# Kernel optimization log

Hardware: AMD Instinct MI355X
Metric: run time of the kernel (lower is better)

Reference implementation:

```python
import jax, jax.numpy as jnp
import numpy as np

EMB_DIM = 64
TREE_DIM = 128
VOCAB = 10000
SORT_VOCAB = 64
DEPTH = 8  # levels 0..8; leaves are level 0, root is level DEPTH
N_TREES = 256


def _tree_topology(depth):
    # perfect binary tree, nodes laid out leaves-first so the root is the LAST node
    level_sizes = [2 ** (depth - l) for l in range(depth + 1)]
    offsets = np.cumsum([0] + level_sizes)
    n = int(offsets[-1])  # 2^(depth+1)-1
    node_order = np.concatenate([np.full(level_sizes[l], l, np.int64) for l in range(depth + 1)])
    par, chi, eo = [], [], []
    for l in range(1, depth + 1):
        p = offsets[l] + np.arange(level_sizes[l])
        c0 = offsets[l - 1] + 2 * np.arange(level_sizes[l])
        par.append(np.repeat(p, 2))
        chi.append(np.stack([c0, c0 + 1], 1).reshape(-1))
        eo.append(np.full(2 * level_sizes[l], l, np.int64))
    return n, node_order, np.concatenate(par), np.concatenate(chi), np.concatenate(eo)


def setup_inputs():
    key = jax.random.key(0)
    ks = jax.random.split(key, 16)
    n, no, par, chi, eo = _tree_topology(DEPTH)
    offs = np.arange(N_TREES, dtype=np.int64) * n
    node_order = jnp.asarray(np.tile(no, N_TREES))
    parent_idx = jnp.asarray((par[None, :] + offs[:, None]).reshape(-1))
    child_idx = jnp.asarray((chi[None, :] + offs[:, None]).reshape(-1))
    edge_order = jnp.asarray(np.tile(eo, N_TREES))
    NT = N_TREES * n
    in_dim = 3 * EMB_DIM  # token_emb | sort_emb | const_emb

    def nrm(k, shape, s=0.05):
        return jax.random.normal(k, shape, jnp.float32) * s

    return dict(
        tokens_a=jax.random.randint(ks[0], (NT,), 0, VOCAB * 2),
        sorts_a=jax.random.randint(ks[1], (NT,), 0, SORT_VOCAB * 2),
        const_a=nrm(ks[2], (NT, EMB_DIM), 1.0),
        tokens_b=jax.random.randint(ks[3], (NT,), 0, VOCAB * 2),
        sorts_b=jax.random.randint(ks[4], (NT,), 0, SORT_VOCAB * 2),
        const_b=nrm(ks[5], (NT, EMB_DIM), 1.0),
        node_order=node_order, parent_idx=parent_idx, child_idx=child_idx,
        edge_order=edge_order, n_levels=DEPTH + 1, n_trees=N_TREES,
        emb=nrm(ks[6], (VOCAB * 2, EMB_DIM), 1.0),
        sort_emb_tab=nrm(ks[7], (SORT_VOCAB * 2, EMB_DIM), 1.0),
        W_iou=nrm(ks[8], (in_dim, 3 * TREE_DIM)),
        b_iou=jnp.zeros((3 * TREE_DIM,), jnp.float32),
        U_iou=nrm(ks[9], (TREE_DIM, 3 * TREE_DIM)),
        W_f=nrm(ks[10], (in_dim, TREE_DIM)),
        b_f=jnp.zeros((TREE_DIM,), jnp.float32),
        U_f=nrm(ks[11], (TREE_DIM, TREE_DIM)),
        fc1_w=nrm(ks[12], (2 * TREE_DIM + 1, TREE_DIM)),
        fc1_b=jnp.zeros((TREE_DIM,), jnp.float32),
        fc2_w=nrm(ks[13], (TREE_DIM, 2)),
        fc2_b=jnp.zeros((2,), jnp.float32),
    )


def _treelstm(feat, node_order, parent_idx, child_idx, edge_order, n_levels,
              W_iou, b_iou, U_iou, W_f, b_f, U_f):
    # child-sum TreeLSTM, level-synchronous from leaves (level 0) to root.
    N = feat.shape[0]
    td = U_f.shape[0]
    h = jnp.zeros((N, td), feat.dtype)
    c = jnp.zeros((N, td), feat.dtype)
    wiou_x = feat @ W_iou + b_iou  # [N, 3*td], hoisted out of the level loop
    wf_x = feat @ W_f + b_f        # [N, td]
    for t in range(n_levels):
        nmask = (node_order == t)[:, None]
        emask = (edge_order == t)[:, None].astype(feat.dtype)
        ch = h[child_idx]  # [E, td]
        cc = c[child_idx]
        h_sum = jax.ops.segment_sum(ch * emask, parent_idx, num_segments=N)
        f = jax.nn.sigmoid(wf_x[parent_idx] + ch @ U_f)  # per-edge forget gate
        c_sum = jax.ops.segment_sum(f * cc * emask, parent_idx, num_segments=N)
        i, o, u = jnp.split(wiou_x + h_sum @ U_iou, 3, axis=1)
        c_new = jax.nn.sigmoid(i) * jnp.tanh(u) + c_sum
        h_new = jax.nn.sigmoid(o) * jnp.tanh(c_new)
        h = jnp.where(nmask, h_new, h)
        c = jnp.where(nmask, c_new, c)
    return h, c


def reference(tokens_a, sorts_a, const_a, tokens_b, sorts_b, const_b,
              node_order, parent_idx, child_idx, edge_order, n_levels, n_trees,
              emb, sort_emb_tab, W_iou, b_iou, U_iou, W_f, b_f, U_f,
              fc1_w, fc1_b, fc2_w, fc2_b):
    def tree_root_h(tokens, sorts, const):
        feat = jnp.concatenate([emb[tokens], sort_emb_tab[sorts], const], axis=1)
        h, _ = _treelstm(feat, node_order, parent_idx, child_idx, edge_order,
                         n_levels, W_iou, b_iou, U_iou, W_f, b_f, U_f)
        n_per = h.shape[0] // n_trees
        roots = jnp.arange(n_trees) * n_per + (n_per - 1)  # stack_last_h: root is last node
        return h[roots]
    ha = tree_root_h(tokens_a, sorts_a, const_a)  # [B, td]
    hb = tree_root_h(tokens_b, sorts_b, const_b)
    dotp = jnp.sum(ha * hb, axis=-1, keepdims=True)  # diag(ha @ hb.T)
    hcat = jnp.concatenate([ha, hb, dotp], axis=-1)  # [B, 2*td+1]
    logits = jax.nn.relu(hcat @ fc1_w + fc1_b) @ fc2_w + fc2_b  # [B, 2]
    return logits
```

## Files before the change

kernel.cpp:

```cpp
#include <hip/hip_runtime.h>
#include <stdint.h>
#include <stddef.h>

typedef unsigned short u16;
typedef unsigned long long u64;
typedef short bf16x8 __attribute__((ext_vector_type(8)));
typedef float f32x4 __attribute__((ext_vector_type(4)));

#define NTREES 256
#define NPT 511
#define TD 128
#define PLANE_E ((size_t)65536 * TD)

#define S_TOKA 0
#define S_SRTA 1
#define S_CSTA 2
#define S_TOKB 3
#define S_SRTB 4
#define S_CSTB 5
#define S_EMB  6
#define S_SORT 7
#define S_WIOU 8
#define S_BIOU 9
#define S_UIOU 10
#define S_WF   11
#define S_BF   12
#define S_UF   13
#define S_W1   14
#define S_B1   15
#define S_W2   16
#define S_B2   17

#define O_WIOU 0
#define O_WF   73728
#define O_UIOU 98304
#define O_UF   147456
#define O_BIOU 163840
#define O_BF   164224
#define O_W1   164352
#define O_B1   197248
#define O_W2   197376
#define O_B2   197632
#define W_TOTAL 197634

struct ArgPack { u64 p[32]; int sz[32]; int n; };

static __device__ __forceinline__ float bf2f(u16 x){
  union { unsigned u; float f; } v; v.u = ((unsigned)x) << 16; return v.f;
}
static __device__ __forceinline__ u16 f2bf(float f){
  union { float f; unsigned u; } v; v.f = f;
  unsigned r = v.u + 0x7fffu + ((v.u >> 16) & 1u);
  return (u16)(r >> 16);
}
static __device__ __forceinline__ float sigm(float x){ return 1.f/(1.f+expf(-x)); }
static __device__ __forceinline__ float ldin(const void* p, size_t i, int fl){
  return fl ? ((const float*)p)[i] : bf2f(((const u16*)p)[i]);
}
static __device__ __forceinline__ int ldint(const void* p, size_t i, int i64){
  return ((const int*)p)[i << i64];
}

__global__ void resolve_k(ArgPack ap, u64* __restrict__ tab, int* __restrict__ flags){
  if (threadIdx.x != 0 || blockIdx.x != 0) return;
  if (ap.n >= 24) {
    const int map[18] = {0,1,2,3,4,5,12,13,14,15,16,17,18,19,20,21,22,23};
    for (int s = 0; s < 18; ++s) tab[s] = ap.p[map[s]];
  } else if (ap.n >= 22) {
    const int map[18] = {0,1,2,3,4,5,10,11,12,13,14,15,16,17,18,19,20,21};
    for (int s = 0; s < 18; ++s) tab[s] = ap.p[map[s]];
  }
  int ntok = 0, nsrt = 0, ncst = 0, nb128 = 0;
  int tok_i64 = 0, srt_i64 = 0;
  for (int i = 0; i < ap.n && i < 32; ++i) {
    const int s = ap.sz[i];
    const u64 p = ap.p[i];
    int slot = -1;
    if (s == 8372224)      { slot = ncst ? S_CSTB : S_CSTA; ncst++; }
    else if (s == 130816) {
      const int* q = (const int*)p;
      int nz = 0;
      for (int j = 300; j < 430; ++j) if (q[2 * j + 1] != 0) nz++;
      const int w = (nz == 0) ? 1 : 0;
      long vmax = 0;
      for (int j = 256; j < 768; ++j) { long v = w ? (long)q[2 * j] : (long)q[j]; if (v > vmax) vmax = v; }
      if (vmax <= 16)        slot = -1;
      else if (vmax <= 4096) { slot = nsrt ? S_SRTB : S_SRTA; nsrt++; srt_i64 = w; }
      else                   { slot = ntok ? S_TOKB : S_TOKA; ntok++; tok_i64 = w; }
    }
    else if (s == 1280000) slot = S_EMB;
    else if (s == 8192)    slot = S_SORT;
    else if (s == 73728)   slot = S_WIOU;
    else if (s == 384)     slot = S_BIOU;
    else if (s == 49152)   slot = S_UIOU;
    else if (s == 24576)   slot = S_WF;
    else if (s == 128)     { slot = nb128 ? S_B1 : S_BF; nb128++; }
    else if (s == 16384)   slot = S_UF;
    else if (s == 32896)   slot = S_W1;
    else if (s == 256)     slot = S_W2;
    else if (s == 2)       slot = S_B2;
    if (slot >= 0) tab[slot] = p;
  }
  flags[1] = tok_i64;
  flags[2] = srt_i64;
  const u16* pu = (const u16*)tab[S_EMB];
  int huge = 0;
  for (int i = 0; i < 1024; ++i) { const float v = fabsf(bf2f(pu[2 * i])); if (v > 1e4f) huge++; }
  flags[0] = (huge > 40) ? 1 : 0;
}

__global__ __launch_bounds__(256) void prep_k(const u64* __restrict__ tab,
    const int* __restrict__ flags, float* __restrict__ wf)
{
  const int fl = flags[0];
  const int tid = blockIdx.x * 256 + threadIdx.x;
  if (tid >= W_TOTAL) return;
  float v;
  if      (tid < O_WF)   v = ldin((const void*)tab[S_WIOU], tid - O_WIOU, fl);
  else if (tid < O_UIOU) v = ldin((const void*)tab[S_WF],   tid - O_WF,   fl);
  else if (tid < O_UF)   v = ldin((const void*)tab[S_UIOU], tid - O_UIOU, fl);
  else if (tid < O_BIOU) v = ldin((const void*)tab[S_UF],   tid - O_UF,   fl);
  else if (tid < O_BF)   v = ldin((const void*)tab[S_BIOU], tid - O_BIOU, fl);
  else if (tid < O_W1)   v = ldin((const void*)tab[S_BF],   tid - O_BF,   fl);
  else if (tid < O_B1)   v = ldin((const void*)tab[S_W1],   tid - O_W1,   fl);
  else if (tid < O_W2)   v = ldin((const void*)tab[S_B1],   tid - O_B1,   fl);
  else if (tid < O_B2)   v = ldin((const void*)tab[S_W2],   tid - O_W2,   fl);
  else                   v = ldin((const void*)tab[S_B2],   tid - O_B2,   fl);
  wf[tid] = v;
}

__global__ __launch_bounds__(256) void prep_w(const u64* __restrict__ tab,
    const int* __restrict__ flags, u16* __restrict__ wzhi, u16* __restrict__ wzlo,
    float* __restrict__ bz)
{
  const int fl = flags[0];
  const int tid = blockIdx.x * 256 + threadIdx.x;
  if (tid < 640) {
    bz[tid] = (tid < 384) ? ldin((const void*)tab[S_BIOU], tid, fl)
                          : ldin((const void*)tab[S_BF], (tid - 384) & 127, fl);
  }
  if (tid >= 640 * 448) return;
  const int n = tid / 448, k = tid - n * 448;
  float v;
  if (k < 192) {
    v = (n < 384) ? ldin((const void*)tab[S_WIOU], (size_t)k * 384 + n, fl)
                  : ldin((const void*)tab[S_WF],   (size_t)k * 128 + ((n - 384) & 127), fl);
  } else if (k < 320) {
    const int kk = k - 192;
    v = (n < 384) ? ldin((const void*)tab[S_UIOU], (size_t)kk * 384 + n, fl)
      : (n < 512) ? ldin((const void*)tab[S_UF],   (size_t)kk * 128 + (n - 384), fl) : 0.f;
  } else {
    const int kk = k - 320;
    v = (n < 384) ? ldin((const void*)tab[S_UIOU], (size_t)kk * 384 + n, fl)
      : (n < 512) ? 0.f : ldin((const void*)tab[S_UF], (size_t)kk * 128 + (n - 512), fl);
  }
  const u16 hi = f2bf(v);
  wzhi[(size_t)n * 448 + k] = hi;
  wzlo[(size_t)n * 448 + k] = f2bf(v - bf2f(hi));
}

template<bool LEAF>
__global__ __launch_bounds__(512) void gemm_level_k(
    const u64* __restrict__ tab, const int* __restrict__ flags,
    const u16* __restrict__ wzhi, const u16* __restrict__ wzlo,
    const float* __restrict__ bz,
    u16* __restrict__ hhi, u16* __restrict__ hlo, float* __restrict__ cc,
    const int T, const int soArg, const int slotPerSide)
{
  constexpr int NKS = LEAF ? 6 : 14;
  constexpr int NG  = LEAF ? 3 : 5;
  __shared__ __align__(16) u16 Ah[2][4][64][8];
  __shared__ __align__(16) u16 Al[2][4][64][8];

  const int so = soArg + 3 * blockIdx.y;
  const size_t sb = (size_t)slotPerSide * blockIdx.y * TD;
  u16* hps = hhi + sb;
  u16* lps = hlo + sb;
  float* cps = cc + sb;
  const void* tokens = (const void*)tab[so + 0];
  const void* sorts  = (const void*)tab[so + 1];
  const void* cstp   = (const void*)tab[so + 2];
  const void* emb    = (const void*)tab[S_EMB];
  const void* sortt  = (const void*)tab[S_SORT];
  const int fl = flags[0], ti = flags[1], si = flags[2];
  const int tid = threadIdx.x, l = tid & 63, w = tid >> 6, lr = l & 15, lq = l >> 4;
  const int m0 = blockIdx.x * 64;
  const int lpt = 8 - T, mask = (1 << lpt) - 1, offp = 512 - (1 << (9 - T));

  const int srow = tid & 63, skq = tid >> 6;
  const int sm = m0 + srow;
  const int stree = sm >> lpt, sj = sm & mask;
  const size_t snode = (size_t)stree * NPT + offp + sj;
  int tok = ldint(tokens, snode, ti); tok = tok < 0 ? 0 : (tok > 19999 ? 19999 : tok);
  int srt = ldint(sorts,  snode, si); srt = srt < 0 ? 0 : (srt > 127 ? 127 : srt);
  size_t sc0 = 0, sc1 = 0;
  if (!LEAF) { sc0 = ((size_t)sm) << T; sc1 = sc0 + ((size_t)1 << (T - 1)); }

  auto stage = [&](int ks, int buf) {
    const int kg = ks * 32 + skq * 4;
    u16 hi4[4], lo4[4];
    if (LEAF || kg < 192) {
      if (fl) {
        const float* src;
        if (kg < 64)       src = (const float*)emb   + (size_t)tok * 64 + kg;
        else if (kg < 128) src = (const float*)sortt + (size_t)srt * 64 + (kg - 64);
        else               src = (const float*)cstp  + snode * 64 + (kg - 128);
        const float4 v = *(const float4*)src;
        const float xv[4] = {v.x, v.y, v.z, v.w};
#pragma unroll
        for (int j = 0; j < 4; ++j) {
          hi4[j] = f2bf(xv[j]);
          lo4[j] = f2bf(xv[j] - bf2f(hi4[j]));
        }
      } else {
        const u16* src;
        if (kg < 64)       src = (const u16*)emb   + (size_t)tok * 64 + kg;
        else if (kg < 128) src = (const u16*)sortt + (size_t)srt * 64 + (kg - 64);
        else               src = (const u16*)cstp  + snode * 64 + (kg - 128);
#pragma unroll
        for (int j = 0; j < 4; ++j) { hi4[j] = src[j]; lo4[j] = 0; }
      }
    } else {
      const size_t cslot = (kg < 320) ? sc0 : sc1;
      const int off = (kg < 320) ? (kg - 192) : (kg - 320);
      *(uint2*)hi4 = *(const uint2*)(hps + cslot * TD + off);
      *(uint2*)lo4 = *(const uint2*)(lps + cslot * TD + off);
    }
    *(uint2*)&Ah[buf][skq >> 1][srow][(skq & 1) * 4] = *(const uint2*)hi4;
    *(uint2*)&Al[buf][skq >> 1][srow][(skq & 1) * 4] = *(const uint2*)lo4;
  };

  f32x4 acc[4][NG];
#pragma unroll
  for (int mf = 0; mf < 4; ++mf)
#pragma unroll
    for (int g = 0; g < NG; ++g) acc[mf][g] = f32x4{0.f, 0.f, 0.f, 0.f};

  stage(0, 0);
  for (int ks = 0; ks < NKS; ++ks) {
    __syncthreads();
    if (ks + 1 < NKS) stage(ks + 1, (ks + 1) & 1);
    const int k0 = ks * 32;
    const int buf = ks & 1;
    bf16x8 ah[4], al[4];
#pragma unroll
    for (int mf = 0; mf < 4; ++mf) {
      ah[mf] = *(const bf16x8*)&Ah[buf][lq][mf * 16 + lr][0];
      al[mf] = *(const bf16x8*)&Al[buf][lq][mf * 16 + lr][0];
    }
#pragma unroll
    for (int g = 0; g < NG; ++g) {
      if (!LEAF) {
        if (g == 3 && k0 >= 320) continue;
        if (g == 4 && k0 >= 192 && k0 < 320) continue;
      }
      const size_t boff = (size_t)((g * 8 + w) * 16 + lr) * 448 + k0 + lq * 8;
      const bf16x8 bh = *(const bf16x8*)&wzhi[boff];
      const bf16x8 bl = *(const bf16x8*)&wzlo[boff];
#pragma unroll
      for (int mf = 0; mf < 4; ++mf) {
        acc[mf][g] = __builtin_amdgcn_mfma_f32_16x16x32_bf16(ah[mf], bh, acc[mf][g], 0, 0, 0);
        acc[mf][g] = __builtin_amdgcn_mfma_f32_16x16x32_bf16(al[mf], bh, acc[mf][g], 0, 0, 0);
        acc[mf][g] = __builtin_amdgcn_mfma_f32_16x16x32_bf16(ah[mf], bl, acc[mf][g], 0, 0, 0);
      }
    }
  }

  const int d = w * 16 + lr;
  const float bi = bz[d], bo = bz[128 + d], bu = bz[256 + d];
  float bf0 = 0.f, bf1 = 0.f;
  if (!LEAF) { bf0 = bz[384 + d]; bf1 = bz[512 + d]; }
#pragma unroll
  for (int mf = 0; mf < 4; ++mf) {
#pragma unroll
    for (int rr = 0; rr < 4; ++rr) {
      const int row = mf * 16 + lq * 4 + rr;
      const int m = m0 + row;
      const size_t ps = LEAF ? (size_t)m : (((size_t)m) << T);
      const float iv = acc[mf][0][rr] + bi;
      const float ov = acc[mf][1][rr] + bo;
      const float uv = acc[mf][2][rr] + bu;
      float cn = sigm(iv) * tanhf(uv);
      if (!LEAF) {
        const size_t c1s = ps + ((size_t)1 << (T - 1));
        cn += sigm(acc[mf][3][rr] + bf0) * cps[ps * TD + d]
            + sigm(acc[mf][4][rr] + bf1) * cps[c1s * TD + d];
      }
      cps[ps * TD + d] = cn;
      const float hv = sigm(ov) * tanhf(cn);
      const u16 hh = f2bf(hv);
      hps[ps * TD + d] = hh;
      lps[ps * TD + d] = f2bf(hv - bf2f(hh));
    }
  }
}

template<int L>
__global__ __launch_bounds__(128) void bottom_k(const u64* __restrict__ tab,
    const int* __restrict__ flags, const float* __restrict__ wf,
    float* __restrict__ h, float* __restrict__ c, const int so)
{
  constexpr int G = 16 >> L;
  __shared__ float sfeat[16][192];
  __shared__ float childh[16][128];
  const void* tokens = (const void*)tab[so + 0];
  const void* sorts  = (const void*)tab[so + 1];
  const void* cst    = (const void*)tab[so + 2];
  const void* emb    = (const void*)tab[S_EMB];
  const void* sortt  = (const void*)tab[S_SORT];
  const int d = threadIdx.x;
  const int fl = flags[0], ti = flags[1], si = flags[2];
  const int m0 = blockIdx.x * G;

  const float bi  = wf[O_BIOU + d];
  const float bo  = wf[O_BIOU + 128 + d];
  const float bu  = wf[O_BIOU + 256 + d];
  const float bf_ = wf[O_BF + d];

  for (int idx = d; idx < 16 * 192; idx += 128) {
    const int g = idx / 192, k = idx - g * 192;
    const int gl = (m0 << L) + g;
    const int tree = gl >> 8, j = gl & 255;
    const size_t node = (size_t)tree * NPT + j;
    float v;
    if (k < 64) {
      int tk = ldint(tokens, node, ti); tk = tk < 0 ? 0 : (tk > 19999 ? 19999 : tk);
      v = ldin(emb, (size_t)tk * 64 + k, fl);
    } else if (k < 128) {
      int sr = ldint(sorts, node, si); sr = sr < 0 ? 0 : (sr > 127 ? 127 : sr);
      v = ldin(sortt, (size_t)sr * 64 + (k - 64), fl);
    } else v = ldin(cst, node * 64 + (k - 128), fl);
    sfeat[g][k] = v;
  }
  __syncthreads();

  float hb[16], cb[16];
  {
    float ai[16], ao[16], au[16];
#pragma unroll
    for (int g = 0; g < 16; ++g) { ai[g] = bi; ao[g] = bo; au[g] = bu; }
    for (int k = 0; k < 192; ++k) {
      const float wi = wf[O_WIOU + (size_t)k * 384 + d];
      const float wo = wf[O_WIOU + (size_t)k * 384 + 128 + d];
      const float wu = wf[O_WIOU + (size_t)k * 384 + 256 + d];
#pragma unroll
      for (int g = 0; g < 16; ++g) {
        const float x = sfeat[g][k];
        ai[g] = fmaf(x, wi, ai[g]);
        ao[g] = fmaf(x, wo, ao[g]);
        au[g] = fmaf(x, wu, au[g]);
      }
    }
#pragma unroll
    for (int g = 0; g < 16; ++g) {
      const float cv = sigm(ai[g]) * tanhf(au[g]);
      cb[g] = cv;
      hb[g] = sigm(ao[g]) * tanhf(cv);
    }
  }

#pragma unroll
  for (int lev = 1; lev <= L; ++lev) {
    const int nn = 16 >> lev;
    __syncthreads();
#pragma unroll
    for (int j = 0; j < 32; ++j)
      if (j < 2 * nn) childh[j][d] = hb[j];
    for (int idx = d; idx < nn * 192; idx += 128) {
      const int g = idx / 192, k = idx - g * 192;
      const int gle = (m0 << (L - lev)) + g;
      const int lpt = 8 - lev;
      const int tree = gle >> lpt, j = gle & ((1 << lpt) - 1);
      const size_t node = (size_t)tree * NPT + (512 - (1 << (9 - lev))) + j;
      float v;
      if (k < 64) {
        int tk = ldint(tokens, node, ti); tk = tk < 0 ? 0 : (tk > 19999 ? 19999 : tk);
        v = ldin(emb, (size_t)tk * 64 + k, fl);
      } else if (k < 128) {
        int sr = ldint(sorts, node, si); sr = sr < 0 ? 0 : (sr > 127 ? 127 : sr);
        v = ldin(sortt, (size_t)sr * 64 + (k - 64), fl);
      } else v = ldin(cst, node * 64 + (k - 128), fl);
      sfeat[g][k] = v;
    }
    __syncthreads();

    float ai[8], ao[8], au[8], af[8], f0[8], f1[8];
#pragma unroll
    for (int g = 0; g < 8; ++g) { ai[g] = bi; ao[g] = bo; au[g] = bu; af[g] = bf_; f0[g] = 0.f; f1[g] = 0.f; }
    for (int k = 0; k < 192; ++k) {
      const float wi = wf[O_WIOU + (size_t)k * 384 + d];
      const float wo = wf[O_WIOU + (size_t)k * 384 + 128 + d];
      const float wu = wf[O_WIOU + (size_t)k * 384 + 256 + d];
      const float wfc = wf[O_WF + (size_t)k * 128 + d];
#pragma unroll
      for (int g = 0; g < 8; ++g) {
        if (g < nn) {
          const float x = sfeat[g][k];
          ai[g] = fmaf(x, wi, ai[g]);
          ao[g] = fmaf(x, wo, ao[g]);
          au[g] = fmaf(x, wu, au[g]);
          af[g] = fmaf(x, wfc, af[g]);
        }
      }
    }
    for (int k = 0; k < 128; ++k) {
      const float ui = wf[O_UIOU + (size_t)k * 384 + d];
      const float uo = wf[O_UIOU + (size_t)k * 384 + 128 + d];
      const float uu = wf[O_UIOU + (size_t)k * 384 + 256 + d];
      const float uf = wf[O_UF + (size_t)k * 128 + d];
#pragma unroll
      for (int g = 0; g < 8; ++g) {
        if (g < nn) {
          const float s0 = childh[2 * g][k], s1 = childh[2 * g + 1][k];
          const float s = s0 + s1;
          ai[g] = fmaf(s, ui, ai[g]);
          ao[g] = fmaf(s, uo, ao[g]);
          au[g] = fmaf(s, uu, au[g]);
          f0[g] = fmaf(s0, uf, f0[g]);
          f1[g] = fmaf(s1, uf, f1[g]);
        }
      }
    }
#pragma unroll
    for (int g = 0; g < 8; ++g) {
      if (g < nn) {
        float cn = sigm(ai[g]) * tanhf(au[g])
                 + sigm(af[g] + f0[g]) * cb[2 * g]
                 + sigm(af[g] + f1[g]) * cb[2 * g + 1];
        hb[g] = sigm(ao[g]) * tanhf(cn);
        cb[g] = cn;
      }
    }
  }

#pragma unroll
  for (int g = 0; g < 16; ++g)
    if (g < G) {
      h[((size_t)(m0 + g)) * TD + d] = hb[g];
      c[((size_t)(m0 + g)) * TD + d] = cb[g];
    }
}

__global__ __launch_bounds__(128) void level_k(const u64* __restrict__ tab,
    const int* __restrict__ flags, const float* __restrict__ wf,
    float* __restrict__ h, float* __restrict__ c, const int so,
    const int lpt, const int offp, const int tt)
{
  __shared__ float sf[8][192];
  __shared__ float sh0[8][128], sh1[8][128];
  const void* tokens = (const void*)tab[so + 0];
  const void* sorts  = (const void*)tab[so + 1];
  const void* cst    = (const void*)tab[so + 2];
  const void* emb    = (const void*)tab[S_EMB];
  const void* sortt  = (const void*)tab[S_SORT];
  const int d = threadIdx.x;
  const int fl = flags[0], ti = flags[1], si = flags[2];
  const int m0 = blockIdx.x * 8;
  const int mask = (1 << lpt) - 1;

  for (int idx = d; idx < 8 * 192; idx += 128) {
    const int g = idx / 192, k = idx - g * 192;
    const int m = m0 + g;
    const int tree = m >> lpt, j = m & mask;
    const size_t node = (size_t)tree * NPT + offp + j;
    float v;
    if (k < 64) {
      int tk = ldint(tokens, node, ti); tk = tk < 0 ? 0 : (tk > 19999 ? 19999 : tk);
      v = ldin(emb, (size_t)tk * 64 + k, fl);
    } else if (k < 128) {
      int sr = ldint(sorts, node, si); sr = sr < 0 ? 0 : (sr > 127 ? 127 : sr);
      v = ldin(sortt, (size_t)sr * 64 + (k - 64), fl);
    } else v = ldin(cst, node * 64 + (k - 128), fl);
    sf[g][k] = v;
  }
  for (int idx = d; idx < 8 * 128; idx += 128) {
    const int g = idx >> 7, k = idx & 127;
    const size_t s0 = ((size_t)(m0 + g)) << tt;
    const size_t s1 = s0 + ((size_t)1 << (tt - 1));
    sh0[g][k] = h[s0 * TD + k];
    sh1[g][k] = h[s1 * TD + k];
  }
  __syncthreads();

  const float bi  = wf[O_BIOU + d];
  const float bo  = wf[O_BIOU + 128 + d];
  const float bu  = wf[O_BIOU + 256 + d];
  const float bf_ = wf[O_BF + d];

  float ai[8], ao[8], au[8], af[8], f0[8], f1[8];
#pragma unroll
  for (int g = 0; g < 8; ++g) { ai[g] = bi; ao[g] = bo; au[g] = bu; af[g] = bf_; f0[g] = 0.f; f1[g] = 0.f; }

  for (int k = 0; k < 192; ++k) {
    const float wi = wf[O_WIOU + (size_t)k * 384 + d];
    const float wo = wf[O_WIOU + (size_t)k * 384 + 128 + d];
    const float wu = wf[O_WIOU + (size_t)k * 384 + 256 + d];
    const float wfc = wf[O_WF + (size_t)k * 128 + d];
#pragma unroll
    for (int g = 0; g < 8; ++g) {
      const float x = sf[g][k];
      ai[g] = fmaf(x, wi, ai[g]);
      ao[g] = fmaf(x, wo, ao[g]);
      au[g] = fmaf(x, wu, au[g]);
      af[g] = fmaf(x, wfc, af[g]);
    }
  }
  for (int k = 0; k < 128; ++k) {
    const float ui = wf[O_UIOU + (size_t)k * 384 + d];
    const float uo = wf[O_UIOU + (size_t)k * 384 + 128 + d];
    const float uu = wf[O_UIOU + (size_t)k * 384 + 256 + d];
    const float uf = wf[O_UF + (size_t)k * 128 + d];
#pragma unroll
    for (int g = 0; g < 8; ++g) {
      const float s0 = sh0[g][k], s1 = sh1[g][k], s = s0 + s1;
      ai[g] = fmaf(s,  ui, ai[g]);
      ao[g] = fmaf(s,  uo, ao[g]);
      au[g] = fmaf(s,  uu, au[g]);
      f0[g] = fmaf(s0, uf, f0[g]);
      f1[g] = fmaf(s1, uf, f1[g]);
    }
  }
#pragma unroll
  for (int g = 0; g < 8; ++g) {
    const size_t pslot = ((size_t)(m0 + g)) << tt;
    const size_t s1 = pslot + ((size_t)1 << (tt - 1));
    float cn = sigm(ai[g]) * tanhf(au[g])
             + sigm(af[g] + f0[g]) * c[pslot * TD + d]
             + sigm(af[g] + f1[g]) * c[s1 * TD + d];
    c[pslot * TD + d] = cn;
    h[pslot * TD + d] = sigm(ao[g]) * tanhf(cn);
  }
}

__global__ __launch_bounds__(256) void roots_k(const float* __restrict__ h,
                                               float* __restrict__ ha, const int SH){
  const int gid = blockIdx.x * 256 + threadIdx.x;
  const int tree = gid >> 7, d = gid & 127;
  ha[gid] = h[(((size_t)tree) << SH) * TD + d];
}

__global__ __launch_bounds__(256) void roots_split(const u16* __restrict__ hhi,
    const u16* __restrict__ hlo, float* __restrict__ ha){
  const int gid = blockIdx.x * 256 + threadIdx.x;
  const int tree = gid >> 7, d = gid & 127;
  const size_t idx = (((size_t)tree) << 8) * TD + d;
  ha[gid] = bf2f(hhi[idx]) + bf2f(hlo[idx]);
}

__global__ __launch_bounds__(128) void final_k(const float* __restrict__ ha,
    const float* __restrict__ h, const float* __restrict__ wf,
    const long rb, const int SH, float* __restrict__ out)
{
  __shared__ float sa[128], sb[128], red[2], r0s[2], r1s[2];
  const int t = blockIdx.x, d = threadIdx.x;
  const float av = ha[t * 128 + d];
  const float bv = h[((size_t)rb + (((size_t)t) << SH)) * TD + d];
  sa[d] = av; sb[d] = bv;
  float pdt = av * bv;
#pragma unroll
  for (int off = 32; off; off >>= 1) pdt += __shfl_down(pdt, off);
  if ((d & 63) == 0) red[d >> 6] = pdt;
  __syncthreads();
  const float dotp = red[0] + red[1];
  float r = wf[O_B1 + d];
  for (int k = 0; k < 128; ++k) r = fmaf(sa[k], wf[O_W1 + (size_t)k * 128 + d], r);
  for (int k = 0; k < 128; ++k) r = fmaf(sb[k], wf[O_W1 + (size_t)(128 + k) * 128 + d], r);
  r = fmaf(dotp, wf[O_W1 + (size_t)256 * 128 + d], r);
  r = fmaxf(r, 0.f);
  float o0 = r * wf[O_W2 + (size_t)d * 2];
  float o1 = r * wf[O_W2 + (size_t)d * 2 + 1];
#pragma unroll
  for (int off = 32; off; off >>= 1) { o0 += __shfl_down(o0, off); o1 += __shfl_down(o1, off); }
  if ((d & 63) == 0) { r0s[d >> 6] = o0; r1s[d >> 6] = o1; }
  __syncthreads();
  if (d == 0) {
    out[t * 2]     = r0s[0] + r0s[1] + wf[O_B2];
    out[t * 2 + 1] = r1s[0] + r1s[1] + wf[O_B2 + 1];
  }
}

__global__ __launch_bounds__(128) void final_split(const float* __restrict__ ha,
    const u16* __restrict__ hhi, const u16* __restrict__ hlo,
    const float* __restrict__ wf, const u64 rb, float* __restrict__ out)
{
  __shared__ float sa[128], sb[128], red[2], r0s[2], r1s[2];
  const int t = blockIdx.x, d = threadIdx.x;
  const float av = ha[t * 128 + d];
  const size_t idx = rb + (((size_t)t) << 8) * TD + d;
  const float bv = bf2f(hhi[idx]) + bf2f(hlo[idx]);
  sa[d] = av; sb[d] = bv;
  float pdt = av * bv;
#pragma unroll
  for (int off = 32; off; off >>= 1) pdt += __shfl_down(pdt, off);
  if ((d & 63) == 0) red[d >> 6] = pdt;
  __syncthreads();
  const float dotp = red[0] + red[1];
  float r = wf[O_B1 + d];
  for (int k = 0; k < 128; ++k) r = fmaf(sa[k], wf[O_W1 + (size_t)k * 128 + d], r);
  for (int k = 0; k < 128; ++k) r = fmaf(sb[k], wf[O_W1 + (size_t)(128 + k) * 128 + d], r);
  r = fmaf(dotp, wf[O_W1 + (size_t)256 * 128 + d], r);
  r = fmaxf(r, 0.f);
  float o0 = r * wf[O_W2 + (size_t)d * 2];
  float o1 = r * wf[O_W2 + (size_t)d * 2 + 1];
#pragma unroll
  for (int off = 32; off; off >>= 1) { o0 += __shfl_down(o0, off); o1 += __shfl_down(o1, off); }
  if ((d & 63) == 0) { r0s[d >> 6] = o0; r1s[d >> 6] = o1; }
  __syncthreads();
  if (d == 0) {
    out[t * 2]     = r0s[0] + r0s[1] + wf[O_B2];
    out[t * 2 + 1] = r1s[0] + r1s[1] + wf[O_B2 + 1];
  }
}

static void run_gemm_levels(const u64* tab, const int* flags, const u16* wzhi,
                            const u16* wzlo, const float* bz,
                            u16* hhi, u16* hlo, float* cc,
                            int soArg, int slotPerSide, int nsides, hipStream_t stream)
{
  gemm_level_k<true><<<dim3(1024, nsides), 512, 0, stream>>>(
      tab, flags, wzhi, wzlo, bz, hhi, hlo, cc, 0, soArg, slotPerSide);
  for (int T = 1; T <= 8; ++T) {
    const int blocks = (NTREES << (8 - T)) / 64;
    gemm_level_k<false><<<dim3(blocks, nsides), 512, 0, stream>>>(
        tab, flags, wzhi, wzlo, bz, hhi, hlo, cc, T, soArg, slotPerSide);
  }
}

static void run_side_valu(int L, const u64* tab, const int* flags, const float* wf,
                          float* h, float* c, int so, hipStream_t stream)
{
  const int nb = (NTREES << (8 - L)) / (16 >> L);
  switch (L) {
    case 1: bottom_k<1><<<nb, 128, 0, stream>>>(tab, flags, wf, h, c, so); break;
    case 2: bottom_k<2><<<nb, 128, 0, stream>>>(tab, flags, wf, h, c, so); break;
    case 3: bottom_k<3><<<nb, 128, 0, stream>>>(tab, flags, wf, h, c, so); break;
    default: bottom_k<4><<<nb, 128, 0, stream>>>(tab, flags, wf, h, c, so); break;
  }
  for (int t = L + 1; t <= 8; ++t) {
    const int NL = NTREES << (8 - t);
    level_k<<<NL / 8, 128, 0, stream>>>(tab, flags, wf, h, c, so,
        8 - t, 512 - (1 << (9 - t)), t - L);
  }
}

extern "C" void kernel_launch(void* const* d_in, const int* in_sizes, int n_in,
                              void* d_out, int out_size, void* d_ws, size_t ws_size,
                              hipStream_t stream)
{
  ArgPack ap;
  ap.n = n_in < 32 ? n_in : 32;
  for (int i = 0; i < 32; ++i) {
    ap.p[i]  = (i < n_in) ? (u64)d_in[i] : 0ull;
    ap.sz[i] = (i < n_in) ? in_sizes[i] : 0;
  }

  char* p = (char*)d_ws;
  auto take = [&](size_t bytes){ char* q = p; p += (bytes + 255) & ~(size_t)255; return q; };

  u64*   tab   = (u64*)take(18 * 8);
  int*   flags = (int*)take(256);
  float* wfb   = (float*)take((size_t)W_TOTAL * 4);
  u16*   wzhi  = (u16*)take((size_t)640 * 448 * 2);
  u16*   wzlo  = (u16*)take((size_t)640 * 448 * 2);
  float* bz    = (float*)take(640 * 4);
  float* ha    = (float*)take((size_t)NTREES * TD * 4);
  const size_t fixedB = (size_t)(p - (char*)d_ws);

  const size_t sideB = PLANE_E * (2 + 2 + 4);
  const size_t need_conc = fixedB + 2 * sideB + (1 << 16);
  const size_t need_seq  = fixedB + 1 * sideB + (1 << 16);

  resolve_k<<<1, 64, 0, stream>>>(ap, tab, flags);
  prep_k<<<(W_TOTAL + 255) / 256, 256, 0, stream>>>(tab, flags, wfb);

  if (ws_size >= need_seq) {
    prep_w<<<(640 * 448 + 255) / 256, 256, 0, stream>>>(tab, flags, wzhi, wzlo, bz);
    const int nsides = (ws_size >= need_conc) ? 2 : 1;
    u16*   hhi = (u16*)take((size_t)nsides * PLANE_E * 2);
    u16*   hlo = (u16*)take((size_t)nsides * PLANE_E * 2);
    float* cc  = (float*)take((size_t)nsides * PLANE_E * 4);
    if (nsides == 2) {
      run_gemm_levels(tab, flags, wzhi, wzlo, bz, hhi, hlo, cc, S_TOKA, 65536, 2, stream);
      roots_split<<<(NTREES * TD) / 256, 256, 0, stream>>>(hhi, hlo, ha);
      final_split<<<NTREES, 128, 0, stream>>>(ha, hhi, hlo, wfb, (u64)PLANE_E, (float*)d_out);
    } else {
      run_gemm_levels(tab, flags, wzhi, wzlo, bz, hhi, hlo, cc, S_TOKA, 0, 1, stream);
      roots_split<<<(NTREES * TD) / 256, 256, 0, stream>>>(hhi, hlo, ha);
      run_gemm_levels(tab, flags, wzhi, wzlo, bz, hhi, hlo, cc, S_TOKB, 0, 1, stream);
      final_split<<<NTREES, 128, 0, stream>>>(ha, hhi, hlo, wfb, 0ull, (float*)d_out);
    }
    return;
  }

  int L = 1;
  while (L < 4) {
    const size_t need = fixedB + 2 * (((size_t)(NTREES << (8 - L))) * TD * 4 + 256) + 1024;
    if (ws_size >= need) break;
    ++L;
  }
  const int SH = 8 - L;
  const size_t hcB = ((size_t)(NTREES << SH)) * TD * 4;
  float* h = (float*)take(hcB);
  float* c = (float*)take(hcB);
  run_side_valu(L, tab, flags, wfb, h, c, S_TOKA, stream);
  roots_k<<<(NTREES * TD) / 256, 256, 0, stream>>>(h, ha, SH);
  run_side_valu(L, tab, flags, wfb, h, c, S_TOKB, stream);
  final_k<<<NTREES, 128, 0, stream>>>(ha, h, wfb, 0L, SH, (float*)d_out);
}
```

Baseline: 878.1 us.

## Load GEMM A-fragments directly from global memory, removing LDS staging and barriers

The level GEMM kernel no longer stages A tiles through double-buffered shared memory with per-step __syncthreads. Each lane now computes its own four row indices and loads its 8-element bf16x8 fragments straight from global memory (embeddings, constants or child h planes) into registers, with the k-loop fully unrolled. This removes LDS traffic and barrier stalls. In exchange, each of the 8 waves loads the same A data redundantly, so global/L2 traffic and register pressure rise. The MFMA issue order is also regrouped so the hi*hi, lo*hi and hi*lo passes run as separate loops over the four row fragments.

```diff
diff --git a/kernel.cpp b/kernel.cpp
--- a/kernel.cpp
+++ b/kernel.cpp
@@ -169,8 +169,6 @@
 {
   constexpr int NKS = LEAF ? 6 : 14;
   constexpr int NG  = LEAF ? 3 : 5;
-  __shared__ __align__(16) u16 Ah[2][4][64][8];
-  __shared__ __align__(16) u16 Al[2][4][64][8];
 
   const int so = soArg + 3 * blockIdx.y;
   const size_t sb = (size_t)slotPerSide * blockIdx.y * TD;
@@ -187,66 +185,62 @@
   const int m0 = blockIdx.x * 64;
   const int lpt = 8 - T, mask = (1 << lpt) - 1, offp = 512 - (1 << (9 - T));
 
-  const int srow = tid & 63, skq = tid >> 6;
-  const int sm = m0 + srow;
-  const int stree = sm >> lpt, sj = sm & mask;
-  const size_t snode = (size_t)stree * NPT + offp + sj;
-  int tok = ldint(tokens, snode, ti); tok = tok < 0 ? 0 : (tok > 19999 ? 19999 : tok);
-  int srt = ldint(sorts,  snode, si); srt = srt < 0 ? 0 : (srt > 127 ? 127 : srt);
-  size_t sc0 = 0, sc1 = 0;
-  if (!LEAF) { sc0 = ((size_t)sm) << T; sc1 = sc0 + ((size_t)1 << (T - 1)); }
-
-  auto stage = [&](int ks, int buf) {
-    const int kg = ks * 32 + skq * 4;
-    u16 hi4[4], lo4[4];
-    if (LEAF || kg < 192) {
-      if (fl) {
-        const float* src;
-        if (kg < 64)       src = (const float*)emb   + (size_t)tok * 64 + kg;
-        else if (kg < 128) src = (const float*)sortt + (size_t)srt * 64 + (kg - 64);
-        else               src = (const float*)cstp  + snode * 64 + (kg - 128);
-        const float4 v = *(const float4*)src;
-        const float xv[4] = {v.x, v.y, v.z, v.w};
-#pragma unroll
-        for (int j = 0; j < 4; ++j) {
-          hi4[j] = f2bf(xv[j]);
-          lo4[j] = f2bf(xv[j] - bf2f(hi4[j]));
+  int tok[4], srt[4];
+  size_t nodeA[4], sc0[4], sc1[4];
+#pragma unroll
+  for (int mf = 0; mf < 4; ++mf) {
+    const int m = m0 + mf * 16 + lr;
+    const int tree = m >> lpt, j = m & mask;
+    nodeA[mf] = (size_t)tree * NPT + offp + j;
+    int tk = ldint(tokens, nodeA[mf], ti); tok[mf] = tk < 0 ? 0 : (tk > 19999 ? 19999 : tk);
+    int sr = ldint(sorts,  nodeA[mf], si); srt[mf] = sr < 0 ? 0 : (sr > 127 ? 127 : sr);
+    if (!LEAF) { sc0[mf] = ((size_t)m) << T; sc1[mf] = sc0[mf] + ((size_t)1 << (T - 1)); }
+  }
+
+  f32x4 acc[4][NG];
+#pragma unroll
+  for (int mf = 0; mf < 4; ++mf)
+#pragma unroll
+    for (int g = 0; g < NG; ++g) acc[mf][g] = f32x4{0.f, 0.f, 0.f, 0.f};
+
+#pragma unroll
+  for (int ks = 0; ks < NKS; ++ks) {
+    const int k0 = ks * 32;
+    const int kg = k0 + lq * 8;
+    bf16x8 ah[4], al[4];
+#pragma unroll
+    for (int mf = 0; mf < 4; ++mf) {
+      if (LEAF || kg < 192) {
+        if (fl) {
+          const float* src;
+          if (kg < 64)       src = (const float*)emb   + (size_t)tok[mf] * 64 + kg;
+          else if (kg < 128) src = (const float*)sortt + (size_t)srt[mf] * 64 + (kg - 64);
+          else               src = (const float*)cstp  + nodeA[mf] * 64 + (kg - 128);
+          const float4 v0 = *(const float4*)src;
+          const float4 v1 = *(const float4*)(src + 4);
+          const float xv[8] = {v0.x, v0.y, v0.z, v0.w, v1.x, v1.y, v1.z, v1.w};
+          bf16x8 hh, ll;
+#pragma unroll
+          for (int q = 0; q < 8; ++q) {
+            const u16 hb = f2bf(xv[q]);
+            hh[q] = (short)hb;
+            ll[q] = (short)f2bf(xv[q] - bf2f(hb));
+          }
+          ah[mf] = hh; al[mf] = ll;
+        } else {
+          const u16* src;
+          if (kg < 64)       src = (const u16*)emb   + (size_t)tok[mf] * 64 + kg;
+          else if (kg < 128) src = (const u16*)sortt + (size_t)srt[mf] * 64 + (kg - 64);
+          else               src = (const u16*)cstp  + nodeA[mf] * 64 + (kg - 128);
+          ah[mf] = *(const bf16x8*)src;
+          al[mf] = bf16x8{0,0,0,0,0,0,0,0};
         }
       } else {
-        const u16* src;
-        if (kg < 64)       src = (const u16*)emb   + (size_t)tok * 64 + kg;
-        else if (kg < 128) src = (const u16*)sortt + (size_t)srt * 64 + (kg - 64);
-        else               src = (const u16*)cstp  + snode * 64 + (kg - 128);
-#pragma unroll
-        for (int j = 0; j < 4; ++j) { hi4[j] = src[j]; lo4[j] = 0; }
+        const size_t base = (kg < 320) ? sc0[mf] : sc1[mf];
+        const int off = kg - (kg < 320 ? 192 : 320);
+        ah[mf] = *(const bf16x8*)(hps + base * TD + off);
+        al[mf] = *(const bf16x8*)(lps + base * TD + off);
       }
-    } else {
-      const size_t cslot = (kg < 320) ? sc0 : sc1;
-      const int off = (kg < 320) ? (kg - 192) : (kg - 320);
-      *(uint2*)hi4 = *(const uint2*)(hps + cslot * TD + off);
-      *(uint2*)lo4 = *(const uint2*)(lps + cslot * TD + off);
-    }
-    *(uint2*)&Ah[buf][skq >> 1][srow][(skq & 1) * 4] = *(const uint2*)hi4;
-    *(uint2*)&Al[buf][skq >> 1][srow][(skq & 1) * 4] = *(const uint2*)lo4;
-  };
-
-  f32x4 acc[4][NG];
-#pragma unroll
-  for (int mf = 0; mf < 4; ++mf)
-#pragma unroll
-    for (int g = 0; g < NG; ++g) acc[mf][g] = f32x4{0.f, 0.f, 0.f, 0.f};
-
-  stage(0, 0);
-  for (int ks = 0; ks < NKS; ++ks) {
-    __syncthreads();
-    if (ks + 1 < NKS) stage(ks + 1, (ks + 1) & 1);
-    const int k0 = ks * 32;
-    const int buf = ks & 1;
-    bf16x8 ah[4], al[4];
-#pragma unroll
-    for (int mf = 0; mf < 4; ++mf) {
-      ah[mf] = *(const bf16x8*)&Ah[buf][lq][mf * 16 + lr][0];
-      al[mf] = *(const bf16x8*)&Al[buf][lq][mf * 16 + lr][0];
     }
 #pragma unroll
     for (int g = 0; g < NG; ++g) {
@@ -254,15 +248,18 @@
         if (g == 3 && k0 >= 320) continue;
         if (g == 4 && k0 >= 192 && k0 < 320) continue;
       }
-      const size_t boff = (size_t)((g * 8 + w) * 16 + lr) * 448 + k0 + lq * 8;
+      const size_t boff = (size_t)((g * 8 + w) * 16 + lr) * 448 + kg;
       const bf16x8 bh = *(const bf16x8*)&wzhi[boff];
       const bf16x8 bl = *(const bf16x8*)&wzlo[boff];
 #pragma unroll
-      for (int mf = 0; mf < 4; ++mf) {
+      for (int mf = 0; mf < 4; ++mf)
         acc[mf][g] = __builtin_amdgcn_mfma_f32_16x16x32_bf16(ah[mf], bh, acc[mf][g], 0, 0, 0);
+#pragma unroll
+      for (int mf = 0; mf < 4; ++mf)
         acc[mf][g] = __builtin_amdgcn_mfma_f32_16x16x32_bf16(al[mf], bh, acc[mf][g], 0, 0, 0);
+#pragma unroll
+      for (int mf = 0; mf < 4; ++mf)
         acc[mf][g] = __builtin_amdgcn_mfma_f32_16x16x32_bf16(ah[mf], bl, acc[mf][g], 0, 0, 0);
-      }
     }
   }
 
@@ -277,17 +274,17 @@
       const int row = mf * 16 + lq * 4 + rr;
       const int m = m0 + row;
       const size_t ps = LEAF ? (size_t)m : (((size_t)m) << T);
-      const float iv = acc[mf][0][rr] + bi;
-      const float ov = acc[mf][1][rr] + bo;
-      const float uv = acc[mf][2][rr] + bu;
-      float cn = sigm(iv) * tanhf(uv);
+      const float va = acc[mf][0][rr] + bi;
+      const float vo = acc[mf][1][rr] + bo;
+      const float vu = acc[mf][2][rr] + bu;
+      float cn = sigm(va) * tanhf(vu);
       if (!LEAF) {
         const size_t c1s = ps + ((size_t)1 << (T - 1));
         cn += sigm(acc[mf][3][rr] + bf0) * cps[ps * TD + d]
             + sigm(acc[mf][4][rr] + bf1) * cps[c1s * TD + d];
       }
       cps[ps * TD + d] = cn;
-      const float hv = sigm(ov) * tanhf(cn);
+      const float hv = sigm(vo) * tanhf(cn);
       const u16 hh = f2bf(hv);
       hps[ps * TD + d] = hh;
       lps[ps * TD + d] = f2bf(hv - bf2f(hh));
```

Measured after the change: 1.142 ms. 30.0% more time.
